# Performance work log

Measured on AMD Instinct MI355X. Metric: run time of the kernel, lower is better.

## Reference

```python
import jax, jax.numpy as jnp
import numpy as np

N = 50000      # nodes
NE = 10000     # hyperedges
NNZ = 600000   # incidence pairs
DIN = 128
DOUT = 128
ALPHA_RES = 0.5  # module's residual mixing coefficient


def _glorot(key, shape):
    fan_in, fan_out = shape[1], shape[0]
    lim = float(np.sqrt(6.0 / (fan_in + fan_out)))
    return jax.random.uniform(key, shape, jnp.float32, -lim, lim)


def setup_inputs() -> dict:
    key = jax.random.key(0)
    ks = jax.random.split(key, 9)
    X = jax.random.normal(ks[0], (N, DIN), jnp.float32)
    X0 = jax.random.normal(ks[1], (N, DIN), jnp.float32)
    vertex = jax.random.randint(ks[2], (NNZ,), 0, N)
    edges = jax.random.randint(ks[3], (NNZ,), 0, NE)
    alpha = jax.random.uniform(ks[4], (NNZ,), jnp.float32)
    # single-layer MLPs -> plain Linear weights (out, in) + bias
    W1_w = _glorot(ks[5], (DOUT, DIN))
    W1_b = jnp.zeros((DOUT,), jnp.float32)
    W2_w = _glorot(ks[6], (DOUT, DIN + DOUT))
    W2_b = jnp.zeros((DOUT,), jnp.float32)
    W_w = _glorot(ks[7], (DOUT, DOUT))
    W_b = jnp.zeros((DOUT,), jnp.float32)
    return {"X": X, "vertex": vertex, "edges": edges, "X0": X0, "alpha": alpha,
            "W1_w": W1_w, "W1_b": W1_b, "W2_w": W2_w, "W2_b": W2_b,
            "W_w": W_w, "W_b": W_b}


def reference(X, vertex, edges, X0, alpha, W1_w, W1_b, W2_w, W2_b, W_w, W_b):
    a = alpha[:, None]                                   # [nnz,1]
    # vertex -> edge: gather W1(X) rows, weight, scatter-add over hyperedges
    Xw1 = X @ W1_w.T + W1_b                              # [N, dout]
    Xve = Xw1[vertex] * a                                # [nnz, dout]
    Xe = jax.ops.segment_sum(Xve, edges, num_segments=NE)  # [NE, dout]
    # edge -> vertex: gather edge feats, concat with raw vertex feats, W2, scatter-add
    Xev = jnp.concatenate([X[vertex], Xe[edges]], axis=-1)  # [nnz, din+dout]
    Xev = (Xev @ W2_w.T + W2_b) * a                      # [nnz, dout]
    Xv = jax.ops.segment_sum(Xev, vertex, num_segments=N)  # [N, dout]
    Xr = (1.0 - ALPHA_RES) * Xv + ALPHA_RES * X0         # residual mix
    return Xr @ W_w.T + W_b
```

## Files before the change

### kernel.cpp

```cpp
#include <hip/hip_runtime.h>

#define NV   50000
#define NEV  10000
#define NNZV 600000
#define DIM  128

#define NBKE 157
#define NBKV 196
#define CH2  2048
#define SCAP 7680

#define BPACK_OFF 0
#define WP_OFF    24576
#define BA_OFF    40960
#define A_OFF     41216
#define B_OFF     91264
#define T_OFF     101312
#define XEBF_OFF  1381312
#define BCNTE_OFF 2021312
#define BOFFE_OFF 2021568
#define BCNTV_OFF 2021824
#define BOFFV_OFF 2022080
#define OFFE_OFF  2031328
#define CURE_OFF  2041344
#define OFFV_OFF  2101376
#define CURV_OFF  2151392
#define PV_OFF    2201920
#define PE_OUT_FLOAT_OFF 3200000

typedef __attribute__((ext_vector_type(8))) short bf16x8;
typedef __attribute__((ext_vector_type(4))) float f32x4;

__device__ __forceinline__ unsigned short f2bf(float x){
  unsigned u = __float_as_uint(x);
  u += 0x7fffu + ((u >> 16) & 1u);
  return (unsigned short)(u >> 16);
}
__device__ __forceinline__ float bf2f(unsigned short h){
  return __uint_as_float((unsigned)h << 16);
}

__global__ __launch_bounds__(256) void zero_counts(int* __restrict__ p){
  int t = threadIdx.x;
  #pragma unroll
  for (int r = 0; r < 4; ++r) p[r*256 + t] = 0;
}

__global__ __launch_bounds__(128) void prep1(
        const float* __restrict__ W2w, const float* __restrict__ W2b,
        const float* __restrict__ Ww, float* __restrict__ ws){
  int b = blockIdx.x, o = threadIdx.x;
  if (b < 256){
    float s;
    if (b < 128){
      float acc = 0.f;
      for (int m = 0; m < 128; ++m) acc += Ww[o*128 + m] * W2w[m*256 + b];
      s = 0.5f * acc;
    } else {
      s = 0.5f * Ww[o*128 + (b - 128)];
    }
    int ks = b >> 5, g = (b >> 3) & 3, j = b & 7;
    int ct = o >> 4, lo = o & 15;
    unsigned short* Bp = (unsigned short*)(ws + BPACK_OFF);
    Bp[((size_t)((ks*8 + ct)*64 + g*16 + lo))*8 + j] = f2bf(s);
  } else if (b < 384){
    int m = b - 256;
    float acc = 0.f;
    for (int j = 0; j < 128; ++j) acc += Ww[o*128 + j] * W2w[j*256 + 128 + m];
    ws[T_OFF + m*128 + o] = 0.5f * acc;
  } else {
    float acc = 0.f;
    for (int m = 0; m < 128; ++m) acc += Ww[o*128 + m] * W2b[m];
    ws[BA_OFF + o] = 0.5f * acc;
  }
}

__global__ __launch_bounds__(128) void prep2(
        const float* __restrict__ W1w, const float* __restrict__ W1b,
        float* __restrict__ ws){
  int b = blockIdx.x, o = threadIdx.x;
  const float* C2t = ws + T_OFF;
  if (b < 128){
    float acc = 0.f;
    for (int m = 0; m < 128; ++m) acc += W1w[m*128 + b] * C2t[m*128 + o];
    ws[WP_OFF + b*128 + o] = acc;
  } else {
    float acc = 0.f;
    for (int m = 0; m < 128; ++m) acc += W1b[m] * C2t[m*128 + o];
    ws[BA_OFF + 128 + o] = acc;
  }
}

__global__ __launch_bounds__(256) void count_bucket(
        const int* __restrict__ vertex, const int* __restrict__ edges,
        int* __restrict__ bcntE, int* __restrict__ bcntV){
  __shared__ int hE[256], hV[256];
  int t = threadIdx.x;
  hE[t] = 0; hV[t] = 0;
  __syncthreads();
  int i0 = blockIdx.x * 2048;
  #pragma unroll
  for (int r = 0; r < 8; ++r){
    int i = i0 + r*256 + t;
    if (i < NNZV){
      atomicAdd(&hE[edges[i]  >> 6], 1);
      atomicAdd(&hV[vertex[i] >> 8], 1);
    }
  }
  __syncthreads();
  if (hE[t]) atomicAdd(bcntE + t, hE[t]);
  if (hV[t]) atomicAdd(bcntV + t, hV[t]);
}

__global__ __launch_bounds__(256) void to_bf16(
        const float* __restrict__ src, unsigned short* __restrict__ dst, int n8){
  int i = blockIdx.x*256 + threadIdx.x;
  if (i >= n8) return;
  float4 v0 = ((const float4*)src)[(size_t)i*2];
  float4 v1 = ((const float4*)src)[(size_t)i*2 + 1];
  ushort4 h0, h1;
  h0.x=f2bf(v0.x); h0.y=f2bf(v0.y); h0.z=f2bf(v0.z); h0.w=f2bf(v0.w);
  h1.x=f2bf(v1.x); h1.y=f2bf(v1.y); h1.z=f2bf(v1.z); h1.w=f2bf(v1.w);
  ((ushort4*)dst)[(size_t)i*2]     = h0;
  ((ushort4*)dst)[(size_t)i*2 + 1] = h1;
}

__global__ __launch_bounds__(256) void scan_buckets(
        const int* __restrict__ bcntE, const int* __restrict__ bcntV,
        int* __restrict__ bOffE, int* __restrict__ bOffV,
        int* __restrict__ bcurE, int* __restrict__ bcurV,
        int* __restrict__ offE, int* __restrict__ offV){
  __shared__ int s[256];
  int t = threadIdx.x;
  int c = (t < NBKE) ? bcntE[t] : 0;
  s[t] = c; __syncthreads();
  for (int d = 1; d < 256; d <<= 1){
    int x = (t >= d) ? s[t-d] : 0;
    __syncthreads(); s[t] += x; __syncthreads();
  }
  if (t < NBKE){ bOffE[t] = s[t] - c; bcurE[t] = s[t] - c; }
  if (t == 0){ bOffE[NBKE] = NNZV; offE[NEV] = NNZV; }
  __syncthreads();
  int c2 = (t < NBKV) ? bcntV[t] : 0;
  s[t] = c2; __syncthreads();
  for (int d = 1; d < 256; d <<= 1){
    int x = (t >= d) ? s[t-d] : 0;
    __syncthreads(); s[t] += x; __syncthreads();
  }
  if (t < NBKV){ bOffV[t] = s[t] - c2; bcurV[t] = s[t] - c2; }
  if (t == 0){ bOffV[NBKV] = NNZV; offV[NV] = NNZV; }
}

__global__ __launch_bounds__(256) void fill_binned2(
        const int* __restrict__ vertex, const int* __restrict__ edges,
        const float* __restrict__ alpha,
        int* __restrict__ bcurE, int* __restrict__ bcurV,
        int2* __restrict__ PE, int2* __restrict__ PV){
  __shared__ int histE[256], lofsE[256], gbaseE[256], posE[256];
  __shared__ int histV[256], lofsV[256], gbaseV[256], posV[256];
  __shared__ int ss[256];
  __shared__ int2 stgE[CH2], stgV[CH2];
  int t = threadIdx.x;
  int i0 = blockIdx.x * CH2;
  histE[t] = 0; histV[t] = 0;
  __syncthreads();
  int pkE[8], pkV[8], pa[8];
  #pragma unroll
  for (int r = 0; r < 8; ++r){
    int i = i0 + r*256 + t;
    int pe = -1, pv = -1, ab = 0;
    if (i < NNZV){
      int v = vertex[i], e = edges[i];
      ab = __float_as_int(alpha[i]);
      pe = (e << 16) | v;
      pv = (v << 14) | e;
      atomicAdd(&histE[pe >> 22], 1);
      atomicAdd(&histV[pv >> 22], 1);
    }
    pkE[r] = pe; pkV[r] = pv; pa[r] = ab;
  }
  __syncthreads();
  int cE = histE[t];
  ss[t] = cE; __syncthreads();
  for (int d = 1; d < 256; d <<= 1){
    int x = (t >= d) ? ss[t-d] : 0;
    __syncthreads(); ss[t] += x; __syncthreads();
  }
  lofsE[t] = ss[t] - cE; posE[t] = ss[t] - cE;
  __syncthreads();
  int cV = histV[t];
  ss[t] = cV; __syncthreads();
  for (int d = 1; d < 256; d <<= 1){
    int x = (t >= d) ? ss[t-d] : 0;
    __syncthreads(); ss[t] += x; __syncthreads();
  }
  lofsV[t] = ss[t] - cV; posV[t] = ss[t] - cV;
  __syncthreads();
  #pragma unroll
  for (int r = 0; r < 8; ++r){
    if (pkE[r] != -1){
      int p = atomicAdd(&posE[pkE[r] >> 22], 1);
      stgE[p] = make_int2(pkE[r], pa[r]);
      int q = atomicAdd(&posV[pkV[r] >> 22], 1);
      stgV[q] = make_int2(pkV[r], pa[r]);
    }
  }
  __syncthreads();
  {
    int cnt = histE[t];
    gbaseE[t] = cnt ? atomicAdd(&bcurE[t], cnt) : 0;
    int cnt2 = histV[t];
    gbaseV[t] = cnt2 ? atomicAdd(&bcurV[t], cnt2) : 0;
  }
  __syncthreads();
  int total = min(CH2, NNZV - i0);
  for (int s = t; s < total; s += 256){
    int lo = 0, hi = NBKE - 1;
    while (lo < hi){ int mid = (lo + hi + 1) >> 1; if (lofsE[mid] <= s) lo = mid; else hi = mid - 1; }
    PE[gbaseE[lo] + (s - lofsE[lo])] = stgE[s];
    lo = 0; hi = NBKV - 1;
    while (lo < hi){ int mid = (lo + hi + 1) >> 1; if (lofsV[mid] <= s) lo = mid; else hi = mid - 1; }
    PV[gbaseV[lo] + (s - lofsV[lo])] = stgV[s];
  }
}

__global__ __launch_bounds__(256) void sort_bucket(
        int2* __restrict__ pairs, const int* __restrict__ bOff,
        int* __restrict__ off, float* __restrict__ sums,
        int2* __restrict__ bounce, int kpb, int shift, int nkeys){
  int b = blockIdx.x, t = threadIdx.x;
  int k0 = b * kpb;
  int r0 = bOff[b], r1 = bOff[b+1];
  int m = r1 - r0;
  __shared__ int hist[256], rnk[256], ssc[256];
  __shared__ int2 srt[SCAP];
  for (int q = t; q < kpb; q += 256) hist[q] = 0;
  __syncthreads();
  int px[30], py[30];
  #pragma unroll
  for (int r = 0; r < 30; ++r){
    int s = r*256 + t;
    int x = -1, y = 0;
    if (s < m && m <= SCAP){
      int2 p = pairs[r0 + s];
      x = p.x; y = p.y;
      atomicAdd(&hist[(x >> shift) - k0], 1);
    }
    px[r] = x; py[r] = y;
  }
  if (m > SCAP){
    for (int s = t; s < m; s += 256){
      int2 p = pairs[r0 + s];
      bounce[s] = p;
      atomicAdd(&hist[(p.x >> shift) - k0], 1);
    }
  }
  __syncthreads();
  int c = (t < kpb) ? hist[t] : 0;
  ssc[t] = c; __syncthreads();
  for (int d = 1; d < 256; d <<= 1){
    int x = (t >= d) ? ssc[t-d] : 0;
    __syncthreads(); ssc[t] += x; __syncthreads();
  }
  if (t < kpb){
    rnk[t] = ssc[t] - c;
    int k = k0 + t;
    if (k < nkeys) off[k] = r0 + ssc[t] - c;
  }
  __syncthreads();
  if (m <= SCAP){
    #pragma unroll
    for (int r = 0; r < 30; ++r){
      if (px[r] >= 0){
        int p = atomicAdd(&rnk[(px[r] >> shift) - k0], 1);
        srt[p] = make_int2(px[r], py[r]);
      }
    }
    __syncthreads();
    for (int s = t; s < m; s += 256) pairs[r0 + s] = srt[s];
    if (t < kpb){
      int k = k0 + t;
      if (k < nkeys){
        float sa = 0.f;
        int s0 = ssc[t] - hist[t], s1 = ssc[t];
        for (int s = s0; s < s1; ++s) sa += __int_as_float(srt[s].y);
        sums[k] = sa;
      }
    }
  } else {
    __syncthreads();
    for (int s = t; s < m; s += 256){
      int2 p = bounce[s];
      int q = atomicAdd(&rnk[(p.x >> shift) - k0], 1);
      pairs[r0 + q] = p;
    }
    __syncthreads();
    if (t < kpb){
      int k = k0 + t;
      if (k < nkeys){
        float sa = 0.f;
        int s0 = ssc[t] - hist[t], s1 = ssc[t];
        for (int s = s0; s < s1; ++s) sa += __int_as_float(pairs[r0 + s].y);
        sums[k] = sa;
      }
    }
  }
}

__global__ __launch_bounds__(256) void edge_reduce(
        const unsigned short* __restrict__ Xbf, const int* __restrict__ offE,
        const int2* __restrict__ PE, float* __restrict__ T){
  int w = threadIdx.x >> 6, l = threadIdx.x & 63;
  int e = blockIdx.x*4 + w;
  int s0 = offE[e], s1 = offE[e+1];
  float acc0 = 0.f, acc1 = 0.f;
  int j = s0;
  for (; j + 4 <= s1; j += 4){
    int2 p0 = PE[j], p1 = PE[j+1], p2 = PE[j+2], p3 = PE[j+3];
    int v0 = (p0.x & 0xFFFF) << 7, v1 = (p1.x & 0xFFFF) << 7;
    int v2 = (p2.x & 0xFFFF) << 7, v3 = (p3.x & 0xFFFF) << 7;
    float x00 = bf2f(Xbf[v0 + l]),      x01 = bf2f(Xbf[v0 + 64 + l]);
    float x10 = bf2f(Xbf[v1 + l]),      x11 = bf2f(Xbf[v1 + 64 + l]);
    float x20 = bf2f(Xbf[v2 + l]),      x21 = bf2f(Xbf[v2 + 64 + l]);
    float x30 = bf2f(Xbf[v3 + l]),      x31 = bf2f(Xbf[v3 + 64 + l]);
    float a0 = __int_as_float(p0.y), a1 = __int_as_float(p1.y);
    float a2 = __int_as_float(p2.y), a3 = __int_as_float(p3.y);
    acc0 += a0*x00 + a1*x10 + a2*x20 + a3*x30;
    acc1 += a0*x01 + a1*x11 + a2*x21 + a3*x31;
  }
  for (; j < s1; ++j){
    int2 p = PE[j];
    int v = (p.x & 0xFFFF) << 7;
    float a = __int_as_float(p.y);
    acc0 += a * bf2f(Xbf[v + l]);
    acc1 += a * bf2f(Xbf[v + 64 + l]);
  }
  size_t o = (size_t)e * DIM;
  T[o + l]      = acc0;
  T[o + 64 + l] = acc1;
}

__global__ __launch_bounds__(256) void gemm_ye(float* __restrict__ ws){
  __shared__ float Y[32][136];
  const float* T   = ws + T_OFF;
  const float* WP  = ws + WP_OFF;
  const float* Bs  = ws + B_OFF;
  const float* b1p = ws + BA_OFF + 128;
  unsigned short* Ye = (unsigned short*)(ws + XEBF_OFF);
  int n0 = blockIdx.x * 32;
  int tid = threadIdx.x;
  {
    int lr = tid >> 3, lj = tid & 7;
    int gn = n0 + lr; if (gn >= NEV) gn = NEV - 1;
    const float* src = T + (size_t)gn*DIM + lj*16;
    #pragma unroll
    for (int q = 0; q < 4; ++q)
      *(float4*)(&Y[lr][lj*16 + q*4]) = *(const float4*)(src + q*4);
  }
  __syncthreads();
  int rq = tid >> 5, cq = tid & 31;
  float acc[4][4];
  #pragma unroll
  for (int u=0;u<4;++u){ acc[u][0]=0;acc[u][1]=0;acc[u][2]=0;acc[u][3]=0; }
  const float* Crow = WP + cq*4;
  #pragma unroll 4
  for (int k = 0; k < 128; ++k){
    float4 c = *(const float4*)(Crow + (size_t)k*128);
    #pragma unroll
    for (int u = 0; u < 4; ++u){
      float y = Y[rq*4 + u][k];
      acc[u][0] += y*c.x; acc[u][1] += y*c.y; acc[u][2] += y*c.z; acc[u][3] += y*c.w;
    }
  }
  float4 b1v = *(const float4*)(b1p + cq*4);
  #pragma unroll
  for (int u = 0; u < 4; ++u){
    int e = n0 + rq*4 + u;
    if (e < NEV){
      float Bv = Bs[e];
      ushort4 h;
      h.x = f2bf(acc[u][0] + Bv*b1v.x); h.y = f2bf(acc[u][1] + Bv*b1v.y);
      h.z = f2bf(acc[u][2] + Bv*b1v.z); h.w = f2bf(acc[u][3] + Bv*b1v.w);
      *(ushort4*)(Ye + (size_t)e*DIM + cq*4) = h;
    }
  }
}

#define LDS_STRIDE 264

__global__ __launch_bounds__(256) void gemm_pq(
        const float* __restrict__ X, const float* __restrict__ X0,
        const float* __restrict__ Wb, const float* __restrict__ ws,
        float* __restrict__ R){
  __shared__ unsigned short At[64 * LDS_STRIDE];
  __shared__ float ArS[64];
  const float* Aa = ws + A_OFF;
  const float* bA = ws + BA_OFF;
  const unsigned short* Bpack = (const unsigned short*)(ws + BPACK_OFF);
  int r0 = blockIdx.x * 64;
  int t = threadIdx.x;
  if (t < 64){
    int gn = r0 + t; if (gn >= NV) gn = NV - 1;
    ArS[t] = Aa[gn];
  }
  __syncthreads();
  #pragma unroll
  for (int seg = 0; seg < 2; ++seg){
    const float* src = (seg == 0) ? X : X0;
    #pragma unroll
    for (int i = 0; i < 8; ++i){
      int idx = t + i*256;
      int row = idx >> 5;
      int c4  = idx & 31;
      int gn = r0 + row; if (gn >= NV) gn = NV - 1;
      float4 v = *(const float4*)(src + (size_t)gn*DIM + c4*4);
      if (seg == 0){
        float Ar = ArS[row];
        v.x *= Ar; v.y *= Ar; v.z *= Ar; v.w *= Ar;
      }
      ushort4 h;
      h.x = f2bf(v.x); h.y = f2bf(v.y); h.z = f2bf(v.z); h.w = f2bf(v.w);
      *(ushort4*)(&At[row*LDS_STRIDE + seg*128 + c4*4]) = h;
    }
  }
  __syncthreads();

  int w = t >> 6, l = t & 63;
  int m0 = w * 16;
  int lr = l & 15, lg = l >> 4;
  f32x4 acc[8];
  #pragma unroll
  for (int ct = 0; ct < 8; ++ct) acc[ct] = (f32x4){0.f,0.f,0.f,0.f};

  const unsigned short* arow = &At[(m0 + lr)*LDS_STRIDE + lg*8];
  #pragma unroll
  for (int ks = 0; ks < 8; ++ks){
    bf16x8 af = *(const bf16x8*)(arow + ks*32);
    const bf16x8* bp = (const bf16x8*)(Bpack) + (size_t)ks*8*64 + l;
    #pragma unroll
    for (int ct = 0; ct < 8; ++ct){
      bf16x8 bf = bp[ct*64];
      acc[ct] = __builtin_amdgcn_mfma_f32_16x16x32_bf16(af, bf, acc[ct], 0, 0, 0);
    }
  }

  #pragma unroll
  for (int ct = 0; ct < 8; ++ct){
    int o = ct*16 + lr;
    float ba = bA[o], wb = Wb[o];
    #pragma unroll
    for (int r = 0; r < 4; ++r){
      int lrow = m0 + lg*4 + r;
      int row = r0 + lrow;
      if (row < NV){
        float Av = ArS[lrow];
        R[(size_t)row*DIM + o] = acc[ct][r] + Av*ba + wb;
      }
    }
  }
}

__global__ __launch_bounds__(256) void vertex_fused(
        const unsigned short* __restrict__ Ye, const int* __restrict__ offV,
        const int2* __restrict__ PV, float* __restrict__ out){
  int w = threadIdx.x >> 6, l = threadIdx.x & 63;
  int v = blockIdx.x*4 + w;
  int s0 = offV[v], s1 = offV[v+1];
  float acc0 = 0.f, acc1 = 0.f;
  int j = s0;
  for (; j + 4 <= s1; j += 4){
    int2 p0 = PV[j], p1 = PV[j+1], p2 = PV[j+2], p3 = PV[j+3];
    int e0 = (p0.x & 0x3FFF) << 7, e1 = (p1.x & 0x3FFF) << 7;
    int e2 = (p2.x & 0x3FFF) << 7, e3 = (p3.x & 0x3FFF) << 7;
    float y00 = bf2f(Ye[e0 + l]),      y01 = bf2f(Ye[e0 + 64 + l]);
    float y10 = bf2f(Ye[e1 + l]),      y11 = bf2f(Ye[e1 + 64 + l]);
    float y20 = bf2f(Ye[e2 + l]),      y21 = bf2f(Ye[e2 + 64 + l]);
    float y30 = bf2f(Ye[e3 + l]),      y31 = bf2f(Ye[e3 + 64 + l]);
    float a0 = __int_as_float(p0.y), a1 = __int_as_float(p1.y);
    float a2 = __int_as_float(p2.y), a3 = __int_as_float(p3.y);
    acc0 += a0*y00 + a1*y10 + a2*y20 + a3*y30;
    acc1 += a0*y01 + a1*y11 + a2*y21 + a3*y31;
  }
  for (; j < s1; ++j){
    int2 p = PV[j];
    int e = (p.x & 0x3FFF) << 7;
    float a = __int_as_float(p.y);
    acc0 += a * bf2f(Ye[e + l]);
    acc1 += a * bf2f(Ye[e + 64 + l]);
  }
  size_t o = (size_t)v * DIM;
  out[o + l]      += acc0;
  out[o + 64 + l] += acc1;
}

extern "C" void kernel_launch(void* const* d_in, const int* in_sizes, int n_in,
                              void* d_out, int out_size, void* d_ws, size_t ws_size,
                              hipStream_t stream){
  const float* X    = (const float*)d_in[0];
  const int*  vertex= (const int*)  d_in[1];
  const int*  edges = (const int*)  d_in[2];
  const float* X0   = (const float*)d_in[3];
  const float* alpha= (const float*)d_in[4];
  const float* W1w  = (const float*)d_in[5];
  const float* W1b  = (const float*)d_in[6];
  const float* W2w  = (const float*)d_in[7];
  const float* W2b  = (const float*)d_in[8];
  const float* Ww   = (const float*)d_in[9];
  const float* Wb   = (const float*)d_in[10];
  float* out = (float*)d_out;
  float* ws  = (float*)d_ws;

  int* bcntE = (int*)(ws + BCNTE_OFF);
  int* bOffE = (int*)(ws + BOFFE_OFF);
  int* bcntV = (int*)(ws + BCNTV_OFF);
  int* bOffV = (int*)(ws + BOFFV_OFF);
  int* offE  = (int*)(ws + OFFE_OFF);
  int* bcurE = (int*)(ws + CURE_OFF);
  int* offV  = (int*)(ws + OFFV_OFF);
  int* bcurV = (int*)(ws + CURV_OFF);
  int2* PV   = (int2*)(ws + PV_OFF);
  int2* PE   = (int2*)(out + PE_OUT_FLOAT_OFF);
  int2* bounce = (int2*)(ws + T_OFF);
  unsigned short* Xbf = (unsigned short*)out;
  unsigned short* Ye  = (unsigned short*)(ws + XEBF_OFF);

  zero_counts  <<<1, 256, 0, stream>>>(bcntE);
  prep1        <<<385, 128, 0, stream>>>(W2w, W2b, Ww, ws);
  prep2        <<<129, 128, 0, stream>>>(W1w, W1b, ws);
  count_bucket <<<(NNZV + 2047)/2048, 256, 0, stream>>>(vertex, edges, bcntE, bcntV);
  to_bf16      <<<(NV*DIM/8 + 255)/256, 256, 0, stream>>>(X, Xbf, NV*DIM/8);
  scan_buckets <<<1, 256, 0, stream>>>(bcntE, bcntV, bOffE, bOffV, bcurE, bcurV, offE, offV);
  fill_binned2 <<<(NNZV + CH2 - 1)/CH2, 256, 0, stream>>>(vertex, edges, alpha,
                                                          bcurE, bcurV, PE, PV);
  sort_bucket  <<<NBKE, 256, 0, stream>>>(PE, bOffE, offE, ws + B_OFF, bounce, 64,  16, NEV);
  sort_bucket  <<<NBKV, 256, 0, stream>>>(PV, bOffV, offV, ws + A_OFF, bounce, 256, 14, NV);
  edge_reduce  <<<NEV/4, 256, 0, stream>>>(Xbf, offE, PE, ws + T_OFF);
  gemm_ye      <<<(NEV + 31)/32, 256, 0, stream>>>(ws);
  gemm_pq      <<<(NV + 63)/64, 256, 0, stream>>>(X, X0, Wb, ws, out);
  vertex_fused <<<NV/4, 256, 0, stream>>>(Ye, offV, PV, out);
}
```

Before: 189.2 us.

## Fuse edge bucket sort with edge reduction and merge small setup kernels

The edge-side bucket sort and the per-edge gather-reduce now run in one kernel: each block sorts its 64-edge bucket in LDS and immediately reduces bf16 vertex rows for those edges, so sorted pairs and offsets are never written back to global memory. zero_counts is folded into prep1 and count_bucket is merged with the bf16 conversion, cutting the kernel launch count. The cost is that edge reduction now runs on only 157 blocks instead of 2500, which lowers parallelism for the gather-heavy step. There is also a slow fallback path for oversized buckets.

```diff
diff --git a/kernel.cpp b/kernel.cpp
--- a/kernel.cpp
+++ b/kernel.cpp
@@ -7,6 +7,7 @@
 
 #define NBKE 157
 #define NBKV 196
+#define NCB  293
 #define CH2  2048
 #define SCAP 7680
 
@@ -21,9 +22,8 @@
 #define BOFFE_OFF 2021568
 #define BCNTV_OFF 2021824
 #define BOFFV_OFF 2022080
-#define OFFE_OFF  2031328
+#define OFFV_OFF  2101376
 #define CURE_OFF  2041344
-#define OFFV_OFF  2101376
 #define CURV_OFF  2151392
 #define PV_OFF    2201920
 #define PE_OUT_FLOAT_OFF 3200000
@@ -38,12 +38,6 @@
 }
 __device__ __forceinline__ float bf2f(unsigned short h){
   return __uint_as_float((unsigned)h << 16);
-}
-
-__global__ __launch_bounds__(256) void zero_counts(int* __restrict__ p){
-  int t = threadIdx.x;
-  #pragma unroll
-  for (int r = 0; r < 4; ++r) p[r*256 + t] = 0;
 }
 
 __global__ __launch_bounds__(128) void prep1(
@@ -68,10 +62,14 @@
     float acc = 0.f;
     for (int j = 0; j < 128; ++j) acc += Ww[o*128 + j] * W2w[j*256 + 128 + m];
     ws[T_OFF + m*128 + o] = 0.5f * acc;
-  } else {
+  } else if (b == 384){
     float acc = 0.f;
     for (int m = 0; m < 128; ++m) acc += Ww[o*128 + m] * W2b[m];
     ws[BA_OFF + o] = 0.5f * acc;
+  } else {
+    int* z = (int*)(ws + BCNTE_OFF);
+    int base = (b - 385)*256;
+    z[base + o] = 0; z[base + 128 + o] = 0;
   }
 }
 
@@ -91,45 +89,47 @@
   }
 }
 
-__global__ __launch_bounds__(256) void count_bucket(
+__global__ __launch_bounds__(256) void count_tobf16(
         const int* __restrict__ vertex, const int* __restrict__ edges,
-        int* __restrict__ bcntE, int* __restrict__ bcntV){
+        const float* __restrict__ X,
+        int* __restrict__ bcntE, int* __restrict__ bcntV,
+        unsigned short* __restrict__ Xbf){
+  int b = blockIdx.x, t = threadIdx.x;
   __shared__ int hE[256], hV[256];
-  int t = threadIdx.x;
-  hE[t] = 0; hV[t] = 0;
-  __syncthreads();
-  int i0 = blockIdx.x * 2048;
-  #pragma unroll
-  for (int r = 0; r < 8; ++r){
-    int i = i0 + r*256 + t;
-    if (i < NNZV){
-      atomicAdd(&hE[edges[i]  >> 6], 1);
-      atomicAdd(&hV[vertex[i] >> 8], 1);
-    }
-  }
-  __syncthreads();
-  if (hE[t]) atomicAdd(bcntE + t, hE[t]);
-  if (hV[t]) atomicAdd(bcntV + t, hV[t]);
-}
-
-__global__ __launch_bounds__(256) void to_bf16(
-        const float* __restrict__ src, unsigned short* __restrict__ dst, int n8){
-  int i = blockIdx.x*256 + threadIdx.x;
-  if (i >= n8) return;
-  float4 v0 = ((const float4*)src)[(size_t)i*2];
-  float4 v1 = ((const float4*)src)[(size_t)i*2 + 1];
-  ushort4 h0, h1;
-  h0.x=f2bf(v0.x); h0.y=f2bf(v0.y); h0.z=f2bf(v0.z); h0.w=f2bf(v0.w);
-  h1.x=f2bf(v1.x); h1.y=f2bf(v1.y); h1.z=f2bf(v1.z); h1.w=f2bf(v1.w);
-  ((ushort4*)dst)[(size_t)i*2]     = h0;
-  ((ushort4*)dst)[(size_t)i*2 + 1] = h1;
+  if (b < NCB){
+    hE[t] = 0; hV[t] = 0;
+    __syncthreads();
+    int i0 = b * 2048;
+    #pragma unroll
+    for (int r = 0; r < 8; ++r){
+      int i = i0 + r*256 + t;
+      if (i < NNZV){
+        atomicAdd(&hE[edges[i]  >> 6], 1);
+        atomicAdd(&hV[vertex[i] >> 8], 1);
+      }
+    }
+    __syncthreads();
+    if (hE[t]) atomicAdd(bcntE + t, hE[t]);
+    if (hV[t]) atomicAdd(bcntV + t, hV[t]);
+  } else {
+    int i = (b - NCB)*256 + t;
+    if (i < NV*DIM/8){
+      float4 v0 = ((const float4*)X)[(size_t)i*2];
+      float4 v1 = ((const float4*)X)[(size_t)i*2 + 1];
+      ushort4 h0, h1;
+      h0.x=f2bf(v0.x); h0.y=f2bf(v0.y); h0.z=f2bf(v0.z); h0.w=f2bf(v0.w);
+      h1.x=f2bf(v1.x); h1.y=f2bf(v1.y); h1.z=f2bf(v1.z); h1.w=f2bf(v1.w);
+      ((ushort4*)Xbf)[(size_t)i*2]     = h0;
+      ((ushort4*)Xbf)[(size_t)i*2 + 1] = h1;
+    }
+  }
 }
 
 __global__ __launch_bounds__(256) void scan_buckets(
         const int* __restrict__ bcntE, const int* __restrict__ bcntV,
         int* __restrict__ bOffE, int* __restrict__ bOffV,
         int* __restrict__ bcurE, int* __restrict__ bcurV,
-        int* __restrict__ offE, int* __restrict__ offV){
+        int* __restrict__ offV){
   __shared__ int s[256];
   int t = threadIdx.x;
   int c = (t < NBKE) ? bcntE[t] : 0;
@@ -139,7 +139,7 @@
     __syncthreads(); s[t] += x; __syncthreads();
   }
   if (t < NBKE){ bOffE[t] = s[t] - c; bcurE[t] = s[t] - c; }
-  if (t == 0){ bOffE[NBKE] = NNZV; offE[NEV] = NNZV; }
+  if (t == 0) bOffE[NBKE] = NNZV;
   __syncthreads();
   int c2 = (t < NBKV) ? bcntV[t] : 0;
   s[t] = c2; __syncthreads();
@@ -224,17 +224,130 @@
   }
 }
 
-__global__ __launch_bounds__(256) void sort_bucket(
+__global__ __launch_bounds__(256) void edge_sort_reduce(
+        const unsigned short* __restrict__ Xbf,
+        const int2* __restrict__ PE, const int* __restrict__ bOffE,
+        float* __restrict__ T, float* __restrict__ Bsum){
+  int b = blockIdx.x, t = threadIdx.x;
+  int k0 = b * 64;
+  int r0 = bOffE[b], r1 = bOffE[b+1];
+  int m = r1 - r0;
+  __shared__ int hist[64], ssc[64], rnk[64];
+  __shared__ int2 srt[SCAP];
+  if (t < 64) hist[t] = 0;
+  __syncthreads();
+  bool inLds = (m <= SCAP);
+  int px[30], py[30];
+  if (inLds){
+    #pragma unroll
+    for (int r = 0; r < 30; ++r){
+      int s = r*256 + t;
+      int x = -1, y = 0;
+      if (s < m){
+        int2 p = PE[r0 + s];
+        x = p.x; y = p.y;
+        atomicAdd(&hist[(x >> 16) - k0], 1);
+      }
+      px[r] = x; py[r] = y;
+    }
+  } else {
+    for (int s = t; s < m; s += 256)
+      atomicAdd(&hist[(PE[r0 + s].x >> 16) - k0], 1);
+  }
+  __syncthreads();
+  if (t < 64) ssc[t] = hist[t];
+  __syncthreads();
+  for (int d = 1; d < 64; d <<= 1){
+    int x = (t >= d && t < 64) ? ssc[t-d] : 0;
+    __syncthreads();
+    if (t < 64) ssc[t] += x;
+    __syncthreads();
+  }
+  if (t < 64) rnk[t] = ssc[t] - hist[t];
+  __syncthreads();
+  if (inLds){
+    #pragma unroll
+    for (int r = 0; r < 30; ++r){
+      if (px[r] != -1){
+        int p = atomicAdd(&rnk[(px[r] >> 16) - k0], 1);
+        srt[p] = make_int2(px[r], py[r]);
+      }
+    }
+  }
+  __syncthreads();
+  if (t < 64){
+    int e = k0 + t;
+    if (e < NEV){
+      float sa = 0.f;
+      if (inLds){
+        int s0 = ssc[t] - hist[t], s1 = ssc[t];
+        for (int s = s0; s < s1; ++s) sa += __int_as_float(srt[s].y);
+      } else {
+        for (int s = 0; s < m; ++s){
+          int2 p = PE[r0 + s];
+          if ((p.x >> 16) == e) sa += __int_as_float(p.y);
+        }
+      }
+      Bsum[e] = sa;
+    }
+  }
+  int w = t >> 6, l = t & 63;
+  for (int le = w; le < 64; le += 4){
+    int e = k0 + le;
+    if (e >= NEV) break;
+    float acc0 = 0.f, acc1 = 0.f;
+    if (inLds){
+      int s0 = ssc[le] - hist[le], s1 = ssc[le];
+      int j = s0;
+      for (; j + 4 <= s1; j += 4){
+        int2 p0 = srt[j], p1 = srt[j+1], p2 = srt[j+2], p3 = srt[j+3];
+        int v0 = (p0.x & 0xFFFF) << 7, v1 = (p1.x & 0xFFFF) << 7;
+        int v2 = (p2.x & 0xFFFF) << 7, v3 = (p3.x & 0xFFFF) << 7;
+        float x00 = bf2f(Xbf[v0 + l]),      x01 = bf2f(Xbf[v0 + 64 + l]);
+        float x10 = bf2f(Xbf[v1 + l]),      x11 = bf2f(Xbf[v1 + 64 + l]);
+        float x20 = bf2f(Xbf[v2 + l]),      x21 = bf2f(Xbf[v2 + 64 + l]);
+        float x30 = bf2f(Xbf[v3 + l]),      x31 = bf2f(Xbf[v3 + 64 + l]);
+        float a0 = __int_as_float(p0.y), a1 = __int_as_float(p1.y);
+        float a2 = __int_as_float(p2.y), a3 = __int_as_float(p3.y);
+        acc0 += a0*x00 + a1*x10 + a2*x20 + a3*x30;
+        acc1 += a0*x01 + a1*x11 + a2*x21 + a3*x31;
+      }
+      for (; j < s1; ++j){
+        int2 p = srt[j];
+        int v = (p.x & 0xFFFF) << 7;
+        float a = __int_as_float(p.y);
+        acc0 += a * bf2f(Xbf[v + l]);
+        acc1 += a * bf2f(Xbf[v + 64 + l]);
+      }
+    } else {
+      for (int s = 0; s < m; ++s){
+        int2 p = PE[r0 + s];
+        if ((p.x >> 16) == e){
+          int v = (p.x & 0xFFFF) << 7;
+          float a = __int_as_float(p.y);
+          acc0 += a * bf2f(Xbf[v + l]);
+          acc1 += a * bf2f(Xbf[v + 64 + l]);
+        }
+      }
+    }
+    size_t o = (size_t)e * DIM;
+    T[o + l]      = acc0;
+    T[o + 64 + l] = acc1;
+  }
+}
+
+__global__ __launch_bounds__(256) void sort_bucketV(
         int2* __restrict__ pairs, const int* __restrict__ bOff,
         int* __restrict__ off, float* __restrict__ sums,
-        int2* __restrict__ bounce, int kpb, int shift, int nkeys){
+        int2* __restrict__ bounce){
+  const int kpb = 256, shift = 14, nkeys = NV;
   int b = blockIdx.x, t = threadIdx.x;
   int k0 = b * kpb;
   int r0 = bOff[b], r1 = bOff[b+1];
   int m = r1 - r0;
   __shared__ int hist[256], rnk[256], ssc[256];
   __shared__ int2 srt[SCAP];
-  for (int q = t; q < kpb; q += 256) hist[q] = 0;
+  hist[t] = 0;
   __syncthreads();
   int px[30], py[30];
   #pragma unroll
@@ -256,14 +369,14 @@
     }
   }
   __syncthreads();
-  int c = (t < kpb) ? hist[t] : 0;
+  int c = hist[t];
   ssc[t] = c; __syncthreads();
   for (int d = 1; d < 256; d <<= 1){
     int x = (t >= d) ? ssc[t-d] : 0;
     __syncthreads(); ssc[t] += x; __syncthreads();
   }
-  if (t < kpb){
-    rnk[t] = ssc[t] - c;
+  rnk[t] = ssc[t] - c;
+  {
     int k = k0 + t;
     if (k < nkeys) off[k] = r0 + ssc[t] - c;
   }
@@ -278,7 +391,7 @@
     }
     __syncthreads();
     for (int s = t; s < m; s += 256) pairs[r0 + s] = srt[s];
-    if (t < kpb){
+    {
       int k = k0 + t;
       if (k < nkeys){
         float sa = 0.f;
@@ -295,7 +408,7 @@
       pairs[r0 + q] = p;
     }
     __syncthreads();
-    if (t < kpb){
+    {
       int k = k0 + t;
       if (k < nkeys){
         float sa = 0.f;
@@ -305,39 +418,6 @@
       }
     }
   }
-}
-
-__global__ __launch_bounds__(256) void edge_reduce(
-        const unsigned short* __restrict__ Xbf, const int* __restrict__ offE,
-        const int2* __restrict__ PE, float* __restrict__ T){
-  int w = threadIdx.x >> 6, l = threadIdx.x & 63;
-  int e = blockIdx.x*4 + w;
-  int s0 = offE[e], s1 = offE[e+1];
-  float acc0 = 0.f, acc1 = 0.f;
-  int j = s0;
-  for (; j + 4 <= s1; j += 4){
-    int2 p0 = PE[j], p1 = PE[j+1], p2 = PE[j+2], p3 = PE[j+3];
-    int v0 = (p0.x & 0xFFFF) << 7, v1 = (p1.x & 0xFFFF) << 7;
-    int v2 = (p2.x & 0xFFFF) << 7, v3 = (p3.x & 0xFFFF) << 7;
-    float x00 = bf2f(Xbf[v0 + l]),      x01 = bf2f(Xbf[v0 + 64 + l]);
-    float x10 = bf2f(Xbf[v1 + l]),      x11 = bf2f(Xbf[v1 + 64 + l]);
-    float x20 = bf2f(Xbf[v2 + l]),      x21 = bf2f(Xbf[v2 + 64 + l]);
-    float x30 = bf2f(Xbf[v3 + l]),      x31 = bf2f(Xbf[v3 + 64 + l]);
-    float a0 = __int_as_float(p0.y), a1 = __int_as_float(p1.y);
-    float a2 = __int_as_float(p2.y), a3 = __int_as_float(p3.y);
-    acc0 += a0*x00 + a1*x10 + a2*x20 + a3*x30;
-    acc1 += a0*x01 + a1*x11 + a2*x21 + a3*x31;
-  }
-  for (; j < s1; ++j){
-    int2 p = PE[j];
-    int v = (p.x & 0xFFFF) << 7;
-    float a = __int_as_float(p.y);
-    acc0 += a * bf2f(Xbf[v + l]);
-    acc1 += a * bf2f(Xbf[v + 64 + l]);
-  }
-  size_t o = (size_t)e * DIM;
-  T[o + l]      = acc0;
-  T[o + 64 + l] = acc1;
 }
 
 __global__ __launch_bounds__(256) void gemm_ye(float* __restrict__ ws){
@@ -514,7 +594,6 @@
   int* bOffE = (int*)(ws + BOFFE_OFF);
   int* bcntV = (int*)(ws + BCNTV_OFF);
   int* bOffV = (int*)(ws + BOFFV_OFF);
-  int* offE  = (int*)(ws + OFFE_OFF);
   int* bcurE = (int*)(ws + CURE_OFF);
   int* offV  = (int*)(ws + OFFV_OFF);
   int* bcurV = (int*)(ws + CURV_OFF);
@@ -524,18 +603,16 @@
   unsigned short* Xbf = (unsigned short*)out;
   unsigned short* Ye  = (unsigned short*)(ws + XEBF_OFF);
 
-  zero_counts  <<<1, 256, 0, stream>>>(bcntE);
-  prep1        <<<385, 128, 0, stream>>>(W2w, W2b, Ww, ws);
-  prep2        <<<129, 128, 0, stream>>>(W1w, W1b, ws);
-  count_bucket <<<(NNZV + 2047)/2048, 256, 0, stream>>>(vertex, edges, bcntE, bcntV);
-  to_bf16      <<<(NV*DIM/8 + 255)/256, 256, 0, stream>>>(X, Xbf, NV*DIM/8);
-  scan_buckets <<<1, 256, 0, stream>>>(bcntE, bcntV, bOffE, bOffV, bcurE, bcurV, offE, offV);
-  fill_binned2 <<<(NNZV + CH2 - 1)/CH2, 256, 0, stream>>>(vertex, edges, alpha,
-                                                          bcurE, bcurV, PE, PV);
-  sort_bucket  <<<NBKE, 256, 0, stream>>>(PE, bOffE, offE, ws + B_OFF, bounce, 64,  16, NEV);
-  sort_bucket  <<<NBKV, 256, 0, stream>>>(PV, bOffV, offV, ws + A_OFF, bounce, 256, 14, NV);
-  edge_reduce  <<<NEV/4, 256, 0, stream>>>(Xbf, offE, PE, ws + T_OFF);
-  gemm_ye      <<<(NEV + 31)/32, 256, 0, stream>>>(ws);
-  gemm_pq      <<<(NV + 63)/64, 256, 0, stream>>>(X, X0, Wb, ws, out);
-  vertex_fused <<<NV/4, 256, 0, stream>>>(Ye, offV, PV, out);
-}
+  prep1          <<<389, 128, 0, stream>>>(W2w, W2b, Ww, ws);
+  prep2          <<<129, 128, 0, stream>>>(W1w, W1b, ws);
+  count_tobf16   <<<NCB + (NV*DIM/8 + 255)/256, 256, 0, stream>>>(vertex, edges, X,
+                                                                  bcntE, bcntV, Xbf);
+  scan_buckets   <<<1, 256, 0, stream>>>(bcntE, bcntV, bOffE, bOffV, bcurE, bcurV, offV);
+  fill_binned2   <<<(NNZV + CH2 - 1)/CH2, 256, 0, stream>>>(vertex, edges, alpha,
+                                                            bcurE, bcurV, PE, PV);
+  edge_sort_reduce<<<NBKE, 256, 0, stream>>>(Xbf, PE, bOffE, ws + T_OFF, ws + B_OFF);
+  gemm_ye        <<<(NEV + 31)/32, 256, 0, stream>>>(ws);
+  sort_bucketV   <<<NBKV, 256, 0, stream>>>(PV, bOffV, offV, ws + A_OFF, bounce);
+  gemm_pq        <<<(NV + 63)/64, 256, 0, stream>>>(X, X0, Wb, ws, out);
+  vertex_fused   <<<NV/4, 256, 0, stream>>>(Ye, offV, PV, out);
+}
```

New measurement: 256.8 us. 35.7% more time.
